# Kernel tuning notes

Hardware: AMD Instinct MI355X
Metric: run time of the kernel (lower is better)

The kernel has to match this reference:

```python
import jax, jax.numpy as jnp
import numpy as np
import math

B, L, D, K = 16, 8192, 256, 320
BN_EPS = 1e-5


def setup_inputs() -> dict:
    key = jax.random.key(0)
    k1, k2, k3, k4 = jax.random.split(key, 4)
    x = jax.random.normal(k1, (B, L, D), dtype=jnp.float32)
    bn_weight = 1.0 + 0.1 * jax.random.normal(k2, (D,), dtype=jnp.float32)
    bn_bias = 0.1 * jax.random.normal(k3, (D,), dtype=jnp.float32)
    # xavier_uniform for Embedding(numCodes, codeDim)
    a = math.sqrt(6.0 / (K + D))
    codebook = jax.random.uniform(k4, (K, D), minval=-a, maxval=a, dtype=jnp.float32)
    return {"x": x, "bn_weight": bn_weight, "bn_bias": bn_bias, "codebook": codebook}


def batchnorm1d(x, weight, bias):
    # BatchNorm1d in training mode: stats over (batch, length) per channel,
    # biased variance for normalization (matches torch).
    mean = jnp.mean(x, axis=(0, 1))
    var = jnp.var(x, axis=(0, 1))
    return (x - mean) * jax.lax.rsqrt(var + BN_EPS) * weight + bias


def reference(x, bn_weight, bn_bias, codebook):
    xb = batchnorm1d(x, bn_weight, bn_bias)            # [B, L, D]
    flat = xb.reshape(-1, D)                           # [B*L, D]
    # squared euclidean distance (same argmin as torch.cdist)
    d2 = (jnp.sum(flat * flat, axis=-1, keepdims=True)
          - 2.0 * flat @ codebook.T
          + jnp.sum(codebook * codebook, axis=-1))     # [B*L, K]
    indices = jnp.argmin(d2, axis=-1)                  # [B*L]
    codes = codebook[indices].reshape(B, L, D)         # gather nearest codes
    return codes, indices.reshape(B, L, 1)
```

## Files before the change

### kernel.cpp

```cpp
#include <hip/hip_runtime.h>
#include <hip/hip_bf16.h>

#define NROW 131072
#define D 256
#define K 320
#define BN_EPS 1e-5f
#define FIXSCALE 16777216.0f

typedef _Float16 half8 __attribute__((ext_vector_type(8)));
typedef float f32x4 __attribute__((ext_vector_type(4)));
typedef __attribute__((address_space(3))) unsigned int lds_u32;
typedef __attribute__((address_space(1))) const unsigned int g_u32;


__global__ __launch_bounds__(256) void k_stats_partial(const float* __restrict__ x,
                                                       unsigned long long* __restrict__ acc) {
  const int d = threadIdx.x;
  const int blk = blockIdx.x;
  const float* p = x + (size_t)blk * 256 * D + d;
  float s = 0.f, q = 0.f;
  #pragma unroll 4
  for (int r = 0; r < 256; ++r) {
    float v = p[(size_t)r * D];
    s += v;
    q = fmaf(v, v, q);
  }
  long long si = llrintf(s * FIXSCALE);
  long long qi = llrintf(q * FIXSCALE);
  atomicAdd(&acc[d],       (unsigned long long)si);
  atomicAdd(&acc[256 + d], (unsigned long long)qi);
}

__global__ __launch_bounds__(256) void k_stats_final(const unsigned long long* __restrict__ acc,
                                                     const float* __restrict__ cb,
                                                     float* __restrict__ meanb,
                                                     float* __restrict__ rsb,
                                                     float* __restrict__ cnorm) {
  const int t = threadIdx.x;
  if (blockIdx.x == 0) {
    double s = (double)(long long)acc[t]       / (double)FIXSCALE;
    double q = (double)(long long)acc[256 + t] / (double)FIXSCALE;
    double mean = s / (double)NROW;
    double var  = q / (double)NROW - mean * mean;
    meanb[t] = (float)mean;
    rsb[t]   = (float)(1.0 / sqrt(var + (double)BN_EPS));
  } else {
    for (int code = t; code < K; code += 256) {
      const float* c = cb + (size_t)code * D;
      float s = 0.f;
      for (int dd = 0; dd < D; ++dd) s = fmaf(c[dd], c[dd], s);
      cnorm[code] = s;
    }
  }
}

__global__ __launch_bounds__(64) void k_cbprep(const float* __restrict__ cb,
                                               _Float16* __restrict__ cbx,
                                               unsigned long long* __restrict__ acc) {
  const int b = blockIdx.x;
  const int l = threadIdx.x;
  if (b == 160) {
    #pragma unroll
    for (int j = 0; j < 8; ++j) acc[j * 64 + l] = 0ull;
    return;
  }
  const int nt = b >> 3;
  const int ks = b & 7;
  const int code = nt * 16 + (l & 15);
  const int d0 = ks * 32 + (l >> 4) * 8;
  const float* src = cb + (size_t)code * D + d0;
  const size_t bh = ((size_t)(nt * 2 + 0) * 8 + ks) * 512 + l * 8;
  const size_t bl = ((size_t)(nt * 2 + 1) * 8 + ks) * 512 + l * 8;
  #pragma unroll
  for (int j = 0; j < 8; ++j) {
    float v = src[j];
    _Float16 h = (_Float16)v;
    _Float16 lo = (_Float16)(v - (float)h);
    cbx[bh + j] = h;
    cbx[bl + j] = lo;
  }
}

__global__ __launch_bounds__(256) void k_main(const float* __restrict__ x,
                                              const float* __restrict__ w,
                                              const float* __restrict__ bias,
                                              const float* __restrict__ cb,
                                              const float* __restrict__ meanb,
                                              const float* __restrict__ rsb,
                                              const float* __restrict__ cnorm,
                                              const _Float16* __restrict__ cbx,
                                              float* __restrict__ out) {
  __shared__ _Float16 Bbuf[2][8192];
  __shared__ float sxs[64];
  __shared__ int bsel[64];

  const int t = threadIdx.x;
  const int lane = t & 63;
  const int wv = t >> 6;
  const int c15 = lane & 15;
  const int g = lane >> 4;
  const int row0 = (int)blockIdx.x * 64;

#define ISSUE(c) {                                                            \
    const char* gp_ = (const char*)cbx + (size_t)(c) * 16384 + wv * 4096      \
                      + (size_t)lane * 16;                                    \
    _Float16* lp_ = Bbuf[(c) & 1] + wv * 2048 + lane * 8;                     \
    __builtin_amdgcn_global_load_lds((g_u32*)(gp_),        (lds_u32*)(lp_),         16, 0, 0); \
    __builtin_amdgcn_global_load_lds((g_u32*)(gp_ + 1024), (lds_u32*)(lp_ + 512),   16, 0, 0); \
    __builtin_amdgcn_global_load_lds((g_u32*)(gp_ + 2048), (lds_u32*)(lp_ + 1024),  16, 0, 0); \
    __builtin_amdgcn_global_load_lds((g_u32*)(gp_ + 3072), (lds_u32*)(lp_ + 1536),  16, 0, 0); \
  }

  ISSUE(0);

  half8 ah[8], al[8];
  float accq = 0.f;
  {
    const int arow = row0 + wv * 16 + c15;
    const int dbase = g * 8;
    const float* xp = x + (size_t)arow * D + dbase;
    #pragma unroll
    for (int ks = 0; ks < 8; ++ks) {
      const int d0 = dbase + ks * 32;
      float4 xa = *(const float4*)(xp + ks * 32);
      float4 xb2 = *(const float4*)(xp + ks * 32 + 4);
      float4 m0 = *(const float4*)(meanb + d0);
      float4 m1 = *(const float4*)(meanb + d0 + 4);
      float4 r0 = *(const float4*)(rsb + d0);
      float4 r1 = *(const float4*)(rsb + d0 + 4);
      float4 w0 = *(const float4*)(w + d0);
      float4 w1 = *(const float4*)(w + d0 + 4);
      float4 b0 = *(const float4*)(bias + d0);
      float4 b1 = *(const float4*)(bias + d0 + 4);
      float o0 = ((xa.x - m0.x) * r0.x) * w0.x + b0.x;
      float o1 = ((xa.y - m0.y) * r0.y) * w0.y + b0.y;
      float o2 = ((xa.z - m0.z) * r0.z) * w0.z + b0.z;
      float o3 = ((xa.w - m0.w) * r0.w) * w0.w + b0.w;
      float o4 = ((xb2.x - m1.x) * r1.x) * w1.x + b1.x;
      float o5 = ((xb2.y - m1.y) * r1.y) * w1.y + b1.y;
      float o6 = ((xb2.z - m1.z) * r1.z) * w1.z + b1.z;
      float o7 = ((xb2.w - m1.w) * r1.w) * w1.w + b1.w;
      accq = fmaf(o0, o0, accq); accq = fmaf(o1, o1, accq);
      accq = fmaf(o2, o2, accq); accq = fmaf(o3, o3, accq);
      accq = fmaf(o4, o4, accq); accq = fmaf(o5, o5, accq);
      accq = fmaf(o6, o6, accq); accq = fmaf(o7, o7, accq);
      _Float16 h;
      h = (_Float16)o0; ah[ks][0] = h; al[ks][0] = (_Float16)(o0 - (float)h);
      h = (_Float16)o1; ah[ks][1] = h; al[ks][1] = (_Float16)(o1 - (float)h);
      h = (_Float16)o2; ah[ks][2] = h; al[ks][2] = (_Float16)(o2 - (float)h);
      h = (_Float16)o3; ah[ks][3] = h; al[ks][3] = (_Float16)(o3 - (float)h);
      h = (_Float16)o4; ah[ks][4] = h; al[ks][4] = (_Float16)(o4 - (float)h);
      h = (_Float16)o5; ah[ks][5] = h; al[ks][5] = (_Float16)(o5 - (float)h);
      h = (_Float16)o6; ah[ks][6] = h; al[ks][6] = (_Float16)(o6 - (float)h);
      h = (_Float16)o7; ah[ks][7] = h; al[ks][7] = (_Float16)(o7 - (float)h);
    }
  }

  {
    float v1 = accq + __shfl_xor(accq, 16);
    float sxrow = v1 + __shfl_xor(v1, 32);
    if (lane < 16) sxs[wv * 16 + lane] = sxrow;
  }
  __syncthreads();

  float bv[4];
  int   bix[4];
  #pragma unroll
  for (int r = 0; r < 4; ++r) { bv[r] = 3.4e38f; bix[r] = 0x7fffffff; }

  float sxr[4];
  #pragma unroll
  for (int r = 0; r < 4; ++r) sxr[r] = sxs[wv * 16 + g * 4 + r];

  for (int c = 0; c < 20; ++c) {
    if (c + 1 < 20) ISSUE(c + 1);

    {
      const _Float16* bb = Bbuf[c & 1] + lane * 8;
      f32x4 acc = (f32x4){0.f, 0.f, 0.f, 0.f};
      #pragma unroll
      for (int ks = 0; ks < 8; ++ks) {
        half8 bh = *(const half8*)(bb + ks * 512);
        half8 bl = *(const half8*)(bb + 4096 + ks * 512);
        acc = __builtin_amdgcn_mfma_f32_16x16x32_f16(ah[ks], bh, acc, 0, 0, 0);
        acc = __builtin_amdgcn_mfma_f32_16x16x32_f16(ah[ks], bl, acc, 0, 0, 0);
        acc = __builtin_amdgcn_mfma_f32_16x16x32_f16(al[ks], bh, acc, 0, 0, 0);
      }
      const int code = c * 16 + c15;
      const float cn = cnorm[code];
      #pragma unroll
      for (int r = 0; r < 4; ++r) {
        const float d2 = (sxr[r] - 2.0f * acc[r]) + cn;
        if (d2 < bv[r] || (d2 == bv[r] && code < bix[r])) { bv[r] = d2; bix[r] = code; }
      }
    }
    if (c < 19) __syncthreads();
  }

  #pragma unroll
  for (int off = 8; off >= 1; off >>= 1) {
    #pragma unroll
    for (int r = 0; r < 4; ++r) {
      const float ov = __shfl_xor(bv[r], off);
      const int   oi = __shfl_xor(bix[r], off);
      if (ov < bv[r] || (ov == bv[r] && oi < bix[r])) { bv[r] = ov; bix[r] = oi; }
    }
  }
  if (c15 == 0) {
    #pragma unroll
    for (int r = 0; r < 4; ++r) {
      const int row = wv * 16 + g * 4 + r;
      bsel[row] = bix[r];
      out[(size_t)NROW * D + row0 + row] = (float)bix[r];
    }
  }
  __syncthreads();

  {
    const int lr = t >> 2;
    const int q = t & 3;
    const int code = bsel[lr];
    const float* cp = cb + (size_t)code * D;
    float* op = out + (size_t)(row0 + lr) * D;
    #pragma unroll
    for (int e = 0; e < 16; ++e) {
      *(float4*)(op + e * 16 + q * 4) = *(const float4*)(cp + e * 16 + q * 4);
    }
  }
#undef ISSUE
}

extern "C" void kernel_launch(void* const* d_in, const int* in_sizes, int n_in,
                              void* d_out, int out_size, void* d_ws, size_t ws_size,
                              hipStream_t stream) {
  const float* x    = (const float*)d_in[0];
  const float* w    = (const float*)d_in[1];
  const float* bias = (const float*)d_in[2];
  const float* cb   = (const float*)d_in[3];
  float* out = (float*)d_out;

  unsigned long long* acc = (unsigned long long*)d_ws;
  float* meanb = (float*)((char*)d_ws + 4096);
  float* rsb   = meanb + 256;
  float* cnorm = rsb + 256;
  _Float16* cbx = (_Float16*)((char*)d_ws + 8192);

  k_cbprep<<<161, 64, 0, stream>>>(cb, cbx, acc);
  k_stats_partial<<<512, 256, 0, stream>>>(x, acc);
  k_stats_final<<<2, 256, 0, stream>>>(acc, cb, meanb, rsb, cnorm);
  k_main<<<NROW / 64, 256, 0, stream>>>(x, w, bias, cb, meanb, rsb, cnorm, cbx, out);
}
```

Baseline: 171.9 us.

## Vectorize stats reduction, double block rows, stage codebook via registers

The stats kernel now has each thread load float4 across four channels over slabs of rows and uses fewer blocks, so loads are wider and there are fewer launches' worth of atomics per channel. The main kernel grows to 512 threads covering 128 rows per block, so each codebook chunk staged in LDS is shared by twice as many rows. Codebook staging switches from direct global-to-LDS loads to a register-staged prefetch two chunks ahead. This trades more registers and LDS write instructions for halved codebook traffic per row. The partially shown loop and epilogue indexing is assumed to scale with the block size.

```diff
diff --git a/kernel.cpp b/kernel.cpp
--- a/kernel.cpp
+++ b/kernel.cpp
@@ -9,26 +9,32 @@
 
 typedef _Float16 half8 __attribute__((ext_vector_type(8)));
 typedef float f32x4 __attribute__((ext_vector_type(4)));
-typedef __attribute__((address_space(3))) unsigned int lds_u32;
-typedef __attribute__((address_space(1))) const unsigned int g_u32;
 
 
 __global__ __launch_bounds__(256) void k_stats_partial(const float* __restrict__ x,
                                                        unsigned long long* __restrict__ acc) {
-  const int d = threadIdx.x;
-  const int blk = blockIdx.x;
-  const float* p = x + (size_t)blk * 256 * D + d;
-  float s = 0.f, q = 0.f;
+  const int q = threadIdx.x & 63;
+  const int g2 = threadIdx.x >> 6;
+  const int slab = (int)blockIdx.x * 4 + g2;
+  const float* p = x + (size_t)slab * 256 * D + q * 4;
+  float s0 = 0.f, s1 = 0.f, s2 = 0.f, s3 = 0.f;
+  float q0 = 0.f, q1 = 0.f, q2 = 0.f, q3 = 0.f;
   #pragma unroll 4
   for (int r = 0; r < 256; ++r) {
-    float v = p[(size_t)r * D];
-    s += v;
-    q = fmaf(v, v, q);
-  }
-  long long si = llrintf(s * FIXSCALE);
-  long long qi = llrintf(q * FIXSCALE);
-  atomicAdd(&acc[d],       (unsigned long long)si);
-  atomicAdd(&acc[256 + d], (unsigned long long)qi);
+    float4 v = *(const float4*)(p + (size_t)r * D);
+    s0 += v.x; q0 = fmaf(v.x, v.x, q0);
+    s1 += v.y; q1 = fmaf(v.y, v.y, q1);
+    s2 += v.z; q2 = fmaf(v.z, v.z, q2);
+    s3 += v.w; q3 = fmaf(v.w, v.w, q3);
+  }
+  atomicAdd(&acc[q * 4 + 0],       (unsigned long long)(long long)llrintf(s0 * FIXSCALE));
+  atomicAdd(&acc[q * 4 + 1],       (unsigned long long)(long long)llrintf(s1 * FIXSCALE));
+  atomicAdd(&acc[q * 4 + 2],       (unsigned long long)(long long)llrintf(s2 * FIXSCALE));
+  atomicAdd(&acc[q * 4 + 3],       (unsigned long long)(long long)llrintf(s3 * FIXSCALE));
+  atomicAdd(&acc[256 + q * 4 + 0], (unsigned long long)(long long)llrintf(q0 * FIXSCALE));
+  atomicAdd(&acc[256 + q * 4 + 1], (unsigned long long)(long long)llrintf(q1 * FIXSCALE));
+  atomicAdd(&acc[256 + q * 4 + 2], (unsigned long long)(long long)llrintf(q2 * FIXSCALE));
+  atomicAdd(&acc[256 + q * 4 + 3], (unsigned long long)(long long)llrintf(q3 * FIXSCALE));
 }
 
 __global__ __launch_bounds__(256) void k_stats_final(const unsigned long long* __restrict__ acc,
@@ -81,7 +87,7 @@
   }
 }
 
-__global__ __launch_bounds__(256) void k_main(const float* __restrict__ x,
+__global__ __launch_bounds__(512) void k_main(const float* __restrict__ x,
                                               const float* __restrict__ w,
                                               const float* __restrict__ bias,
                                               const float* __restrict__ cb,
@@ -91,24 +97,27 @@
                                               const _Float16* __restrict__ cbx,
                                               float* __restrict__ out) {
   __shared__ _Float16 Bbuf[2][8192];
-  __shared__ float sxs[64];
-  __shared__ int bsel[64];
+  __shared__ float sxs[128];
+  __shared__ int bsel[128];
 
   const int t = threadIdx.x;
   const int lane = t & 63;
   const int wv = t >> 6;
   const int c15 = lane & 15;
   const int g = lane >> 4;
-  const int row0 = (int)blockIdx.x * 64;
-
-#define ISSUE(c) {                                                            \
-    const char* gp_ = (const char*)cbx + (size_t)(c) * 16384 + wv * 4096      \
-                      + (size_t)lane * 16;                                    \
-    _Float16* lp_ = Bbuf[(c) & 1] + wv * 2048 + lane * 8;                     \
-    __builtin_amdgcn_global_load_lds((g_u32*)(gp_),        (lds_u32*)(lp_),         16, 0, 0); \
-    __builtin_amdgcn_global_load_lds((g_u32*)(gp_ + 1024), (lds_u32*)(lp_ + 512),   16, 0, 0); \
-    __builtin_amdgcn_global_load_lds((g_u32*)(gp_ + 2048), (lds_u32*)(lp_ + 1024),  16, 0, 0); \
-    __builtin_amdgcn_global_load_lds((g_u32*)(gp_ + 3072), (lds_u32*)(lp_ + 1536),  16, 0, 0); \
+  const int row0 = (int)blockIdx.x * 128;
+
+  float4 s0, s1;
+  const char* stg_src = (const char*)cbx + (size_t)t * 16;
+#define ISSUE(c) {                                                  \
+    const char* p_ = stg_src + (size_t)(c) * 16384;                 \
+    s0 = *(const float4*)(p_);                                      \
+    s1 = *(const float4*)(p_ + 8192);                               \
+  }
+#define WRITE(b) {                                                  \
+    char* q_ = (char*)Bbuf[(b)] + t * 16;                           \
+    *(float4*)(q_)        = s0;                                     \
+    *(float4*)(q_ + 8192) = s1;                                     \
   }
 
   ISSUE(0);
@@ -156,6 +165,9 @@
     }
   }
 
+  WRITE(0);
+  ISSUE(1);
+
   {
     float v1 = accq + __shfl_xor(accq, 16);
     float sxrow = v1 + __shfl_xor(v1, 32);
@@ -173,7 +185,8 @@
   for (int r = 0; r < 4; ++r) sxr[r] = sxs[wv * 16 + g * 4 + r];
 
   for (int c = 0; c < 20; ++c) {
-    if (c + 1 < 20) ISSUE(c + 1);
+    if (c + 1 < 20) WRITE((c + 1) & 1);
+    if (c + 2 < 20) ISSUE(c + 2);
 
     {
       const _Float16* bb = Bbuf[c & 1] + lane * 8;
@@ -228,6 +241,7 @@
     }
   }
 #undef ISSUE
+#undef WRITE
 }
 
 extern "C" void kernel_launch(void* const* d_in, const int* in_sizes, int n_in,
@@ -246,7 +260,7 @@
   _Float16* cbx = (_Float16*)((char*)d_ws + 8192);
 
   k_cbprep<<<161, 64, 0, stream>>>(cb, cbx, acc);
-  k_stats_partial<<<512, 256, 0, stream>>>(x, acc);
+  k_stats_partial<<<128, 256, 0, stream>>>(x, acc);
   k_stats_final<<<2, 256, 0, stream>>>(acc, cb, meanb, rsb, cnorm);
-  k_main<<<NROW / 64, 256, 0, stream>>>(x, w, bias, cb, meanb, rsb, cnorm, cbx, out);
-}
+  k_main<<<NROW / 128, 512, 0, stream>>>(x, w, bias, cb, meanb, rsb, cnorm, cbx, out);
+}
```

Result: slower. 214.3 us (+24.6%).
